# Kernel optimization log

Hardware: AMD Instinct MI355X
Metric: run time of the kernel (lower is better)

## Reference

```python
import jax, jax.numpy as jnp
import numpy as np

OUT, IN = 11008, 4096
GROUP = 128
NUM_GROUPS = IN // GROUP  # 32
PACKED = OUT * IN // 2
TOKENS = 4096


def setup_inputs() -> dict:
    key = jax.random.key(0)
    k1, k2, k3, k4 = jax.random.split(key, 4)
    x = jax.random.normal(k1, (TOKENS, IN), dtype=jnp.float32)
    # packed bytes: two int4 values per byte (low nibble = even index)
    w_packed = jax.random.randint(k2, (PACKED,), 0, 256, dtype=jnp.int32)
    # per-(out_channel, group) scale and integer zero-point
    w_scale = jax.random.uniform(k3, (OUT, NUM_GROUPS), dtype=jnp.float32) * 0.02 + 1e-3
    w_zero = jax.random.randint(k4, (OUT, NUM_GROUPS), 0, 16, dtype=jnp.int32)
    return {"x": x, "w_packed": w_packed, "w_scale": w_scale, "w_zero": w_zero}


def _dequant_weight(w_packed, w_scale, w_zero):
    out_features, num_groups = w_scale.shape
    in_features = (w_packed.shape[0] * 2) // out_features
    group = in_features // num_groups
    # unpack nibbles: element 2i -> low nibble, element 2i+1 -> high nibble
    low = w_packed & 15
    high = (w_packed >> 4) & 15
    w4 = jnp.stack([low, high], axis=-1).reshape(out_features, in_features)
    # signed int4: values >= 8 map to value - 16
    w4 = jnp.where(w4 >= 8, w4 - 16, w4).astype(jnp.float32)
    # per-group dequant: (w - zero) * scale
    wg = w4.reshape(out_features, num_groups, group)
    w = (wg - w_zero.astype(jnp.float32)[:, :, None]) * w_scale[:, :, None]
    return w.reshape(out_features, in_features)


def reference(x, w_packed, w_scale, w_zero):
    w = _dequant_weight(w_packed, w_scale, w_zero)  # [OUT, IN]
    return x @ w.T  # [TOKENS, OUT]
```

## Files before the change

### kernel.cpp

```cpp
#include <hip/hip_runtime.h>
#include <stdint.h>
#include <stddef.h>


#define M_TOK 4096
#define K_IN  4096
#define N_OUT 11008
#define NGRP  32

#define MTI 16
#define NTI 43
#define TILES (MTI * NTI)

#define BH_OFF ((size_t)M_TOK * K_IN * 2)

typedef _Float16 h8v __attribute__((ext_vector_type(8)));
typedef float    f4v __attribute__((ext_vector_type(4)));

__device__ __forceinline__ void gload16(const void* g, void* l) {
  __builtin_amdgcn_global_load_lds(
      (__attribute__((address_space(1))) void*)(g),
      (__attribute__((address_space(3))) void*)(l),
      16, 0, 0);
}

#define WAIT_VM4 asm volatile("s_waitcnt vmcnt(4)")
#define BAR __builtin_amdgcn_s_barrier()

__global__ __launch_bounds__(256) void cvt_x_kernel(const float* __restrict__ x,
                                                    _Float16* __restrict__ xh) {
  size_t t = (size_t)blockIdx.x * 256 + threadIdx.x;
  const float4* s = (const float4*)x + t * 2;
  float4 a = s[0], b = s[1];
  h8v o;
  o[0] = (_Float16)a.x; o[1] = (_Float16)a.y; o[2] = (_Float16)a.z; o[3] = (_Float16)a.w;
  o[4] = (_Float16)b.x; o[5] = (_Float16)b.y; o[6] = (_Float16)b.z; o[7] = (_Float16)b.w;
  ((h8v*)xh)[t] = o;
}

__global__ __launch_bounds__(256) void dequant_w_kernel(const int* __restrict__ wp,
                                                        const float* __restrict__ ws,
                                                        const int* __restrict__ wz,
                                                        _Float16* __restrict__ bh) {
  size_t tg = (size_t)blockIdx.x * 256 + threadIdx.x;
  int j   = (int)(tg & 127);
  int row = (int)(tg >> 7);
  int g = j >> 2;
  float s = ws[(size_t)row * NGRP + g];
  float c = -s * (8.0f + (float)wz[(size_t)row * NGRP + g]);
  const int4* src = (const int4*)(wp + (size_t)row * 2048 + j * 16);
  _Float16* dst = bh + (size_t)row * 4096 + j * 32;
#pragma unroll
  for (int b = 0; b < 4; ++b) {
    int4 v = src[b];
    int q[4] = {v.x, v.y, v.z, v.w};
    h8v o;
#pragma unroll
    for (int i = 0; i < 4; ++i) {
      int lo = (q[i] & 15) ^ 8;
      int hi = ((q[i] >> 4) & 15) ^ 8;
      o[2 * i]     = (_Float16)(s * (float)lo + c);
      o[2 * i + 1] = (_Float16)(s * (float)hi + c);
    }
    ((h8v*)dst)[b] = o;
  }
}

__global__ __launch_bounds__(512, 2) void gemm_kernel(
    const _Float16* __restrict__ Ah,
    const _Float16* __restrict__ Bh,
    float* __restrict__ C) {
  __shared__ __align__(128) char smem[131072];

  const int bid = blockIdx.x;
  const int swz = (bid & 7) * 86 + (bid >> 3);
  const int mt = swz / NTI;
  const int nt = swz - mt * NTI;
  const int m0 = mt * 256;
  const int n0 = nt * 256;

  const int tid  = threadIdx.x;
  const int lane = tid & 63;
  const int wid  = tid >> 6;
  const int wm   = wid >> 2;
  const int wn   = wid & 3;
  const int lrow = lane & 15;
  const int quad = lane >> 4;

  const int r0 = wid * 32 + (lane >> 2);
  const int kc = (lane & 3) ^ ((lane >> 3) & 3);
  const size_t gA0 = (size_t)(m0 + r0) * K_IN + kc * 8;
  const size_t gB0 = (size_t)(n0 + r0) * K_IN + kc * 8;
  const int ldsl = wid * 2048;

  const int su   = quad ^ ((lrow >> 1) & 3);
  const int aoff = ((wm * 128 + lrow) * 4 + su) * 16;
  const int boff = 32768 + ((wn * 64 + lrow) * 4 + su) * 16;

  f4v acc[8][4];
#pragma unroll
  for (int i = 0; i < 8; ++i)
#pragma unroll
    for (int j = 0; j < 4; ++j) acc[i][j] = (f4v){0.f, 0.f, 0.f, 0.f};

  h8v af_a[4], af_b[4], bf_a[4], bf_b[4];

#define STAGE4(NXT, KT, KH)                                                    \
  { const _Float16* gA_ = Ah + gA0 + (size_t)(KT) * 64 + (KH) * 32;            \
    const _Float16* gB_ = Bh + gB0 + (size_t)(KT) * 64 + (KH) * 32;            \
    char* lA_ = smem + (NXT) * 65536 + (KH) * 16384 + ldsl;                    \
    gload16(gA_, lA_);                                                         \
    gload16(gA_ + 16 * K_IN, lA_ + 1024);                                      \
    gload16(gB_, lA_ + 32768);                                                 \
    gload16(gB_ + 16 * K_IN, lA_ + 32768 + 1024); }

#define RD_AF(DST, BUF, SEC, MH)                                               \
  { const char* s_ = smem + (BUF) * 65536 + (SEC) * 16384;                     \
    _Pragma("unroll")                                                          \
    for (int i_ = 0; i_ < 4; ++i_)                                             \
      DST[i_] = *(const h8v*)(s_ + aoff + (MH) * 4096 + i_ * 1024); }

#define RD_BF(DST, BUF, SEC)                                                   \
  { const char* s_ = smem + (BUF) * 65536 + (SEC) * 16384;                     \
    _Pragma("unroll")                                                          \
    for (int i_ = 0; i_ < 4; ++i_)                                             \
      DST[i_] = *(const h8v*)(s_ + boff + i_ * 1024); }

#define MFMA16(AF, BF, MH)                                                     \
  { __builtin_amdgcn_s_setprio(1);                                             \
    _Pragma("unroll")                                                          \
    for (int mi_ = 0; mi_ < 4; ++mi_)                                          \
      _Pragma("unroll")                                                        \
      for (int nf_ = 0; nf_ < 4; ++nf_)                                        \
        acc[(MH) * 4 + mi_][nf_] = __builtin_amdgcn_mfma_f32_16x16x32_f16(     \
            AF[mi_], BF[nf_], acc[(MH) * 4 + mi_][nf_], 0, 0, 0);              \
    __builtin_amdgcn_s_setprio(0); }

  STAGE4(0, 0, 0);
  STAGE4(0, 0, 1);
  WAIT_VM4;
  BAR;
  RD_AF(af_a, 0, 0, 0);
  RD_BF(bf_a, 0, 0);

  for (int t = 0; t < 64; t += 2) {
    const int t1 = t + 1;
    const int t2 = (t + 2 < 64) ? t + 2 : 63;
    RD_AF(af_b, 0, 0, 1); STAGE4(1, t1, 0); MFMA16(af_a, bf_a, 0); WAIT_VM4; BAR;
    RD_AF(af_a, 0, 1, 0); RD_BF(bf_b, 0, 1); MFMA16(af_b, bf_a, 1); BAR;
    RD_AF(af_b, 0, 1, 1); STAGE4(1, t1, 1); MFMA16(af_a, bf_b, 0); WAIT_VM4; BAR;
    RD_AF(af_a, 1, 0, 0); RD_BF(bf_a, 1, 0); MFMA16(af_b, bf_b, 1); BAR;
    RD_AF(af_b, 1, 0, 1); STAGE4(0, t2, 0); MFMA16(af_a, bf_a, 0); WAIT_VM4; BAR;
    RD_AF(af_a, 1, 1, 0); RD_BF(bf_b, 1, 1); MFMA16(af_b, bf_a, 1); BAR;
    RD_AF(af_b, 1, 1, 1); STAGE4(0, t2, 1); MFMA16(af_a, bf_b, 0); WAIT_VM4; BAR;
    RD_AF(af_a, 0, 0, 0); RD_BF(bf_a, 0, 0); MFMA16(af_b, bf_b, 1); BAR;
  }

#pragma unroll
  for (int mf = 0; mf < 8; ++mf) {
#pragma unroll
    for (int rr = 0; rr < 4; ++rr) {
      int m = m0 + wm * 128 + mf * 16 + quad * 4 + rr;
      float* crow = C + (size_t)m * N_OUT + n0 + wn * 64 + lrow;
#pragma unroll
      for (int nf = 0; nf < 4; ++nf) crow[nf * 16] = acc[mf][nf][rr];
    }
  }
#undef MFMA16
#undef RD_BF
#undef RD_AF
#undef STAGE4
}

extern "C" void kernel_launch(void* const* d_in, const int* in_sizes, int n_in,
                              void* d_out, int out_size, void* d_ws, size_t ws_size,
                              hipStream_t stream) {
  const float* x   = (const float*)d_in[0];
  const int*   wp  = (const int*)d_in[1];
  const float* wsc = (const float*)d_in[2];
  const int*   wz  = (const int*)d_in[3];

  _Float16* Ah = (_Float16*)d_ws;
  _Float16* Bh = (_Float16*)((char*)d_ws + BH_OFF);

  cvt_x_kernel<<<(M_TOK * (size_t)K_IN) / (8 * 256), 256, 0, stream>>>(x, Ah);
  dequant_w_kernel<<<((size_t)N_OUT * 128) / 256, 256, 0, stream>>>(wp, wsc, wz, Bh);
  gemm_kernel<<<TILES, 512, 0, stream>>>(Ah, Bh, (float*)d_out);
}
```

Measured before the change: 643.1 us.

## Switch GEMM to 32x32x16 MFMA with four-slot LDS pipeline

Replaces the 16x16x32 f16 MFMA tiling with 32x32x16 MFMA fragments, which cuts LDS fragment reads per FLOP and lowers instruction count. The K loop now streams 32-wide K sections through four LDS slots with a prefetch depth of three, one barrier per section. This replaces the double-buffered, half-step schedule. It adds a final vmcnt(0) drain and changes the output store mapping to the 32x32 accumulator layout. Register pressure and per-barrier MFMA work change as well.

```diff
diff --git a/kernel.cpp b/kernel.cpp
--- a/kernel.cpp
+++ b/kernel.cpp
@@ -15,7 +15,7 @@
 #define BH_OFF ((size_t)M_TOK * K_IN * 2)
 
 typedef _Float16 h8v __attribute__((ext_vector_type(8)));
-typedef float    f4v __attribute__((ext_vector_type(4)));
+typedef float    fx16 __attribute__((ext_vector_type(16)));
 
 __device__ __forceinline__ void gload16(const void* g, void* l) {
   __builtin_amdgcn_global_load_lds(
@@ -25,6 +25,7 @@
 }
 
 #define WAIT_VM4 asm volatile("s_waitcnt vmcnt(4)")
+#define WAIT_VM0 asm volatile("s_waitcnt vmcnt(0)")
 #define BAR __builtin_amdgcn_s_barrier()
 
 __global__ __launch_bounds__(256) void cvt_x_kernel(const float* __restrict__ x,
@@ -66,6 +67,8 @@
   }
 }
 
+#define ABASE(S) (((S) >> 1) * 65536 + ((S) & 1) * 16384)
+
 __global__ __launch_bounds__(512, 2) void gemm_kernel(
     const _Float16* __restrict__ Ah,
     const _Float16* __restrict__ Bh,
@@ -84,8 +87,14 @@
   const int wid  = tid >> 6;
   const int wm   = wid >> 2;
   const int wn   = wid & 3;
-  const int lrow = lane & 15;
-  const int quad = lane >> 4;
+
+  const int lrow32 = lane & 31;
+  const int hi     = lane >> 5;
+  const int msk    = (lrow32 >> 1) & 3;
+  const int suk0   = hi ^ msk;
+  const int suk1   = (2 + hi) ^ msk;
+  const int arow   = wm * 128 + lrow32;
+  const int brow   = wn * 64 + lrow32;
 
   const int r0 = wid * 32 + (lane >> 2);
   const int kc = (lane & 3) ^ ((lane >> 3) & 3);
@@ -93,83 +102,87 @@
   const size_t gB0 = (size_t)(n0 + r0) * K_IN + kc * 8;
   const int ldsl = wid * 2048;
 
-  const int su   = quad ^ ((lrow >> 1) & 3);
-  const int aoff = ((wm * 128 + lrow) * 4 + su) * 16;
-  const int boff = 32768 + ((wn * 64 + lrow) * 4 + su) * 16;
-
-  f4v acc[8][4];
-#pragma unroll
-  for (int i = 0; i < 8; ++i)
-#pragma unroll
-    for (int j = 0; j < 4; ++j) acc[i][j] = (f4v){0.f, 0.f, 0.f, 0.f};
-
-  h8v af_a[4], af_b[4], bf_a[4], bf_b[4];
-
-#define STAGE4(NXT, KT, KH)                                                    \
-  { const _Float16* gA_ = Ah + gA0 + (size_t)(KT) * 64 + (KH) * 32;            \
-    const _Float16* gB_ = Bh + gB0 + (size_t)(KT) * 64 + (KH) * 32;            \
-    char* lA_ = smem + (NXT) * 65536 + (KH) * 16384 + ldsl;                    \
+  fx16 acc[4][2];
+#pragma unroll
+  for (int i = 0; i < 4; ++i)
+#pragma unroll
+    for (int j = 0; j < 2; ++j)
+      acc[i][j] = (fx16){0.f,0.f,0.f,0.f,0.f,0.f,0.f,0.f,
+                         0.f,0.f,0.f,0.f,0.f,0.f,0.f,0.f};
+
+  h8v afa[8], afb[8], bfa[4], bfb[4];
+
+#define STG(SLOT, SEC)                                                         \
+  { const _Float16* gA_ = Ah + gA0 + (size_t)(SEC) * 32;                       \
+    const _Float16* gB_ = Bh + gB0 + (size_t)(SEC) * 32;                       \
+    char* lA_ = smem + ABASE(SLOT) + ldsl;                                     \
     gload16(gA_, lA_);                                                         \
     gload16(gA_ + 16 * K_IN, lA_ + 1024);                                      \
     gload16(gB_, lA_ + 32768);                                                 \
     gload16(gB_ + 16 * K_IN, lA_ + 32768 + 1024); }
 
-#define RD_AF(DST, BUF, SEC, MH)                                               \
-  { const char* s_ = smem + (BUF) * 65536 + (SEC) * 16384;                     \
+#define RD_A(DST, SLOT)                                                        \
+  { const char* s_ = smem + ABASE(SLOT);                                       \
     _Pragma("unroll")                                                          \
-    for (int i_ = 0; i_ < 4; ++i_)                                             \
-      DST[i_] = *(const h8v*)(s_ + aoff + (MH) * 4096 + i_ * 1024); }
-
-#define RD_BF(DST, BUF, SEC)                                                   \
-  { const char* s_ = smem + (BUF) * 65536 + (SEC) * 16384;                     \
+    for (int mi_ = 0; mi_ < 4; ++mi_) {                                        \
+      DST[mi_ * 2 + 0] = *(const h8v*)(s_ + ((arow + mi_ * 32) * 4 + suk0) * 16); \
+      DST[mi_ * 2 + 1] = *(const h8v*)(s_ + ((arow + mi_ * 32) * 4 + suk1) * 16); \
+    } }
+
+#define RD_B(DST, SLOT)                                                        \
+  { const char* s_ = smem + ABASE(SLOT) + 32768;                               \
     _Pragma("unroll")                                                          \
-    for (int i_ = 0; i_ < 4; ++i_)                                             \
-      DST[i_] = *(const h8v*)(s_ + boff + i_ * 1024); }
-
-#define MFMA16(AF, BF, MH)                                                     \
+    for (int ni_ = 0; ni_ < 2; ++ni_) {                                        \
+      DST[ni_ * 2 + 0] = *(const h8v*)(s_ + ((brow + ni_ * 32) * 4 + suk0) * 16); \
+      DST[ni_ * 2 + 1] = *(const h8v*)(s_ + ((brow + ni_ * 32) * 4 + suk1) * 16); \
+    } }
+
+#define MM(AF, BF)                                                             \
   { __builtin_amdgcn_s_setprio(1);                                             \
     _Pragma("unroll")                                                          \
-    for (int mi_ = 0; mi_ < 4; ++mi_)                                          \
+    for (int ks_ = 0; ks_ < 2; ++ks_)                                          \
       _Pragma("unroll")                                                        \
-      for (int nf_ = 0; nf_ < 4; ++nf_)                                        \
-        acc[(MH) * 4 + mi_][nf_] = __builtin_amdgcn_mfma_f32_16x16x32_f16(     \
-            AF[mi_], BF[nf_], acc[(MH) * 4 + mi_][nf_], 0, 0, 0);              \
+      for (int mi_ = 0; mi_ < 4; ++mi_)                                        \
+        _Pragma("unroll")                                                      \
+        for (int ni_ = 0; ni_ < 2; ++ni_)                                      \
+          acc[mi_][ni_] = __builtin_amdgcn_mfma_f32_32x32x16_f16(              \
+              AF[mi_ * 2 + ks_], BF[ni_ * 2 + ks_], acc[mi_][ni_], 0, 0, 0);   \
     __builtin_amdgcn_s_setprio(0); }
 
-  STAGE4(0, 0, 0);
-  STAGE4(0, 0, 1);
+  STG(0, 0);
+  STG(1, 1);
+  STG(2, 2);
   WAIT_VM4;
   BAR;
-  RD_AF(af_a, 0, 0, 0);
-  RD_BF(bf_a, 0, 0);
-
-  for (int t = 0; t < 64; t += 2) {
-    const int t1 = t + 1;
-    const int t2 = (t + 2 < 64) ? t + 2 : 63;
-    RD_AF(af_b, 0, 0, 1); STAGE4(1, t1, 0); MFMA16(af_a, bf_a, 0); WAIT_VM4; BAR;
-    RD_AF(af_a, 0, 1, 0); RD_BF(bf_b, 0, 1); MFMA16(af_b, bf_a, 1); BAR;
-    RD_AF(af_b, 0, 1, 1); STAGE4(1, t1, 1); MFMA16(af_a, bf_b, 0); WAIT_VM4; BAR;
-    RD_AF(af_a, 1, 0, 0); RD_BF(bf_a, 1, 0); MFMA16(af_b, bf_b, 1); BAR;
-    RD_AF(af_b, 1, 0, 1); STAGE4(0, t2, 0); MFMA16(af_a, bf_a, 0); WAIT_VM4; BAR;
-    RD_AF(af_a, 1, 1, 0); RD_BF(bf_b, 1, 1); MFMA16(af_b, bf_a, 1); BAR;
-    RD_AF(af_b, 1, 1, 1); STAGE4(0, t2, 1); MFMA16(af_a, bf_b, 0); WAIT_VM4; BAR;
-    RD_AF(af_a, 0, 0, 0); RD_BF(bf_a, 0, 0); MFMA16(af_b, bf_b, 1); BAR;
+  RD_A(afa, 0);
+  RD_B(bfa, 0);
+
+  for (int s = 0; s < 128; s += 4) {
+    const int s4 = (s + 4 < 128) ? s + 4 : 127;
+    const int s5 = (s + 5 < 128) ? s + 5 : 127;
+    const int s6 = (s + 6 < 128) ? s + 6 : 127;
+    RD_A(afb, 1); RD_B(bfb, 1); STG(3, s + 3); MM(afa, bfa); WAIT_VM4; BAR;
+    RD_A(afa, 2); RD_B(bfa, 2); STG(0, s4);    MM(afb, bfb); WAIT_VM4; BAR;
+    RD_A(afb, 3); RD_B(bfb, 3); STG(1, s5);    MM(afa, bfa); WAIT_VM4; BAR;
+    RD_A(afa, 0); RD_B(bfa, 0); STG(2, s6);    MM(afb, bfb); WAIT_VM4; BAR;
   }
-
-#pragma unroll
-  for (int mf = 0; mf < 8; ++mf) {
-#pragma unroll
-    for (int rr = 0; rr < 4; ++rr) {
-      int m = m0 + wm * 128 + mf * 16 + quad * 4 + rr;
-      float* crow = C + (size_t)m * N_OUT + n0 + wn * 64 + lrow;
-#pragma unroll
-      for (int nf = 0; nf < 4; ++nf) crow[nf * 16] = acc[mf][nf][rr];
+  WAIT_VM0;
+
+#pragma unroll
+  for (int mi = 0; mi < 4; ++mi) {
+#pragma unroll
+    for (int ni = 0; ni < 2; ++ni) {
+#pragma unroll
+      for (int r = 0; r < 16; ++r) {
+        int m = m0 + wm * 128 + mi * 32 + (r & 3) + 8 * (r >> 2) + 4 * hi;
+        C[(size_t)m * N_OUT + n0 + wn * 64 + ni * 32 + lrow32] = acc[mi][ni][r];
+      }
     }
   }
-#undef MFMA16
-#undef RD_BF
-#undef RD_AF
-#undef STAGE4
+#undef MM
+#undef RD_B
+#undef RD_A
+#undef STG
 }
 
 extern "C" void kernel_launch(void* const* d_in, const int* in_sizes, int n_in,
```

New measurement: 674.7 us. +4.9%, slower.
